# Optimization experiments

Hardware: AMD Instinct MI355X
Metric: run time of the kernel (lower is better)

The kernel has to match this reference:

```python
import math
import jax, jax.numpy as jnp
import numpy as np

B, S, D, H, F = 2, 2048, 1024, 16, 4096
HD = D // H
EPS = 1e-6
ALPHA, BETA = 0.5, 1.0  # SpectralActivation defaults


def setup_inputs() -> dict:
    key = jax.random.key(0)
    ks = jax.random.split(key, 24)
    init = lambda k, shape: (jax.random.normal(k, shape, jnp.float32) * 0.02)
    return {
        "x": jax.random.normal(ks[0], (B, S, D), jnp.float32),
        # attention params (W stored as [in, out], i.e. y = x @ W + b)
        "Wq": init(ks[1], (D, D)), "bq": jnp.zeros((D,), jnp.float32),
        "Wk": init(ks[2], (D, D)), "bk": jnp.zeros((D,), jnp.float32),
        "Wv": init(ks[3], (D, D)), "bv": jnp.zeros((D,), jnp.float32),
        "Wo": init(ks[4], (D, D)), "bo": jnp.zeros((D,), jnp.float32),
        "resonance": jnp.ones((H, 1, 1), jnp.float32),
        "phase": jnp.zeros((H, 1, 1), jnp.float32),
        # norm1
        "g1": jnp.ones((D,), jnp.float32), "b1": jnp.zeros((D,), jnp.float32),
        "s1": jnp.full((1,), 0.1, jnp.float32),
        # FFN
        "W1": init(ks[5], (D, F)), "bf1": jnp.zeros((F,), jnp.float32),
        "W2": init(ks[6], (F, D)), "bf2": jnp.zeros((D,), jnp.float32),
        # norm2
        "g2": jnp.ones((D,), jnp.float32), "b2": jnp.zeros((D,), jnp.float32),
        "s2": jnp.full((1,), 0.1, jnp.float32),
    }


def _harmonic_ln(x, gamma, beta, stab):
    mean = jnp.mean(x, axis=-1, keepdims=True)
    std = jnp.std(x, axis=-1, keepdims=True, ddof=1)  # torch std is unbiased
    std = std + stab * jnp.sin(std * math.pi)
    return gamma * ((x - mean) / (std + EPS)) + beta


def _spectral_act(x):
    c = math.sqrt(2.0 / math.pi)
    gelu_like = 0.5 * x * (1.0 + jnp.tanh(c * (x + 0.044715 * x ** 3)))
    return gelu_like + ALPHA * jnp.sin(BETA * x)


def _forward(x, Wq, bq, Wk, bk, Wv, bv, Wo, bo, resonance, phase,
             g1, b1, s1, W1, bf1, W2, bf2, g2, b2, s2):
    Bq, Sq, _ = x.shape
    q = (x @ Wq + bq).reshape(Bq, Sq, H, HD).transpose(0, 2, 1, 3)  # [B,H,S,hd]
    k = (x @ Wk + bk).reshape(Bq, Sq, H, HD).transpose(0, 2, 1, 3)
    v = (x @ Wv + bv).reshape(Bq, Sq, H, HD).transpose(0, 2, 1, 3)

    scores = jnp.einsum('bhqd,bhkd->bhqk', q, k) / math.sqrt(HD)  # [B,H,S,S]
    scores = scores + resonance[None] * jnp.sin(scores + phase[None])
    attn = jax.nn.softmax(scores, axis=-1)
    out = jnp.einsum('bhqk,bhkd->bhqd', attn, v)
    out = out.transpose(0, 2, 1, 3).reshape(Bq, Sq, D)
    attn_out = out @ Wo + bo

    x = _harmonic_ln(x + attn_out, g1, b1, s1)
    ff = _spectral_act(x @ W1 + bf1) @ W2 + bf2
    x = _harmonic_ln(x + ff, g2, b2, s2)
    return x


def reference(x, Wq, bq, Wk, bk, Wv, bv, Wo, bo, resonance, phase,
              g1, b1, s1, W1, bf1, W2, bf2, g2, b2, s2):
    return _forward(x, Wq, bq, Wk, bk, Wv, bv, Wo, bo, resonance, phase,
                    g1, b1, s1, W1, bf1, W2, bf2, g2, b2, s2)
```

## Files before the change

### kernel.cpp

```cpp
#include <hip/hip_runtime.h>
#include <cstdint>
#include <cstddef>


typedef float  f32x4  __attribute__((ext_vector_type(4)));
typedef __bf16 bf16x8 __attribute__((ext_vector_type(8)));
typedef unsigned short u16x8 __attribute__((ext_vector_type(8)));
typedef unsigned short u16x4 __attribute__((ext_vector_type(4)));
typedef unsigned int   u32x2 __attribute__((ext_vector_type(2)));
typedef unsigned int   u32x4 __attribute__((ext_vector_type(4)));

#define MFMA_BF16(a, b, c) __builtin_amdgcn_mfma_f32_16x16x32_bf16((a), (b), (c), 0, 0, 0)

static __device__ __forceinline__ unsigned short f32_to_bf16(float f) {
  return __builtin_bit_cast(unsigned short, (__bf16)f);
}
static __device__ __forceinline__ bf16x8 lds_frag(const unsigned short* base, int byte) {
  return __builtin_bit_cast(bf16x8, *(const u16x8*)((const char*)base + byte));
}
static __device__ __forceinline__ float spectral_act(float x) {
  const float c = 0.7978845608028654f;
  float g = 0.5f * x * (1.0f + tanhf(c * (x + 0.044715f * x * x * x)));
  return g + 0.5f * __sinf(x);
}
static __device__ __forceinline__ void gload_lds16(const void* g, void* lds) {
  __builtin_amdgcn_global_load_lds((const __attribute__((address_space(1))) unsigned int*)g,
                                   (__attribute__((address_space(3))) unsigned int*)lds,
                                   16, 0, 0);
}
static __device__ __forceinline__ u32x2 tr_read(unsigned addr) {
  u32x2 r;
  asm volatile("ds_read_b64_tr_b16 %0, %1" : "=v"(r) : "v"(addr));
  return r;
}

__global__ __launch_bounds__(256) void cvt_f32_bf16(const float* __restrict__ in,
                                                    unsigned short* __restrict__ out, int n) {
  int i = (blockIdx.x * 256 + threadIdx.x) * 4;
  if (i < n) {
    float4 v = *(const float4*)(in + i);
    u16x4 o;
    o[0] = f32_to_bf16(v.x); o[1] = f32_to_bf16(v.y);
    o[2] = f32_to_bf16(v.z); o[3] = f32_to_bf16(v.w);
    *(u16x4*)(out + i) = o;
  }
}

__global__ __launch_bounds__(256) void transpose_f32_bf16(const float* __restrict__ W,
                                                          unsigned short* __restrict__ Wt,
                                                          int K, int N) {
  __shared__ float tile[32][33];
  int tx = threadIdx.x & 31, ty = threadIdx.x >> 5;
  int k0 = blockIdx.y * 32, n0 = blockIdx.x * 32;
#pragma unroll
  for (int i = 0; i < 4; i++)
    tile[ty + i * 8][tx] = W[(size_t)(k0 + ty + i * 8) * N + n0 + tx];
  __syncthreads();
#pragma unroll
  for (int i = 0; i < 4; i++)
    Wt[(size_t)(n0 + ty + i * 8) * K + k0 + tx] = f32_to_bf16(tile[tx][ty + i * 8]);
}

template <int BM, int BN, int EPI>
__global__ __launch_bounds__(256) void gemm_bt(const unsigned short* __restrict__ A,
                                               const unsigned short* __restrict__ Bt,
                                               const float* __restrict__ bias,
                                               unsigned short* __restrict__ Cb,
                                               float* __restrict__ Cf,
                                               int M, int N, int K) {
  constexpr int MI = BM / 32;
  constexpr int NI = BN / 32;
  __shared__ unsigned short As[2][BM * 32];
  __shared__ unsigned short Bs[2][BN * 32];
  const int t = threadIdx.x;
  const int lane = t & 63, w = t >> 6;
  const int wr = w >> 1, wc = w & 1;
  const int g = lane >> 4, cc = lane & 15;
  const int row0 = blockIdx.y * BM, col0 = blockIdx.x * BN;

  f32x4 acc[MI][NI];
#pragma unroll
  for (int mi = 0; mi < MI; mi++)
#pragma unroll
    for (int ni = 0; ni < NI; ni++) acc[mi][ni] = (f32x4){0.f, 0.f, 0.f, 0.f};

  const int nk = K >> 5;
  const int srow = lane >> 2;
  const int schunk = (lane & 3) ^ (srow & 3);

  auto stage = [&](int buf, int kt) {
#pragma unroll
    for (int i = 0; i < BM / 64; ++i) {
      int r = i * 64 + w * 16;
      gload_lds16(A + (size_t)(row0 + r + srow) * K + (kt << 5) + schunk * 8,
                  &As[buf][r * 32]);
    }
#pragma unroll
    for (int i = 0; i < BN / 64; ++i) {
      int r = i * 64 + w * 16;
      gload_lds16(Bt + (size_t)(col0 + r + srow) * K + (kt << 5) + schunk * 8,
                  &Bs[buf][r * 32]);
    }
  };

  stage(0, 0);
  __syncthreads();
  int cur = 0;
  for (int kt = 0; kt < nk; ++kt) {
    if (kt + 1 < nk) stage(cur ^ 1, kt + 1);

    bf16x8 af[MI], bg[NI];
#pragma unroll
    for (int mi = 0; mi < MI; mi++) {
      int r = wr * (BM / 2) + mi * 16 + cc;
      af[mi] = lds_frag(&As[cur][0], r * 64 + ((g ^ (cc & 3)) << 4));
    }
#pragma unroll
    for (int ni = 0; ni < NI; ni++) {
      int r = wc * (BN / 2) + ni * 16 + cc;
      bg[ni] = lds_frag(&Bs[cur][0], r * 64 + ((g ^ (cc & 3)) << 4));
    }
#pragma unroll
    for (int mi = 0; mi < MI; mi++)
#pragma unroll
      for (int ni = 0; ni < NI; ni++)
        acc[mi][ni] = MFMA_BF16(af[mi], bg[ni], acc[mi][ni]);

    __syncthreads();
    cur ^= 1;
  }

#pragma unroll
  for (int mi = 0; mi < MI; mi++) {
#pragma unroll
    for (int ni = 0; ni < NI; ni++) {
      int col = col0 + wc * (BN / 2) + ni * 16 + cc;
      float bv = bias[col];
#pragma unroll
      for (int r4 = 0; r4 < 4; r4++) {
        int row = row0 + wr * (BM / 2) + mi * 16 + g * 4 + r4;
        float val = acc[mi][ni][r4] + bv;
        if (EPI == 2) val = spectral_act(val);
        if (EPI == 0 || EPI == 2) Cb[(size_t)row * N + col] = f32_to_bf16(val);
        else                      Cf[(size_t)row * N + col] = val;
      }
    }
  }
}

__global__ __launch_bounds__(256) void attn_fused(const unsigned short* __restrict__ Qb,
                                                  const unsigned short* __restrict__ Kb,
                                                  const unsigned short* __restrict__ Vb,
                                                  int ld,
                                                  const float* __restrict__ resonance,
                                                  const float* __restrict__ phase,
                                                  unsigned short* __restrict__ O, int ldo) {
  constexpr int S = 2048;
  __shared__ unsigned short Ks[64 * 64];
  __shared__ unsigned short Vs[4][64 * 16];
  __shared__ unsigned short Ps[4][16 * 64];

  const int t = threadIdx.x, lane = t & 63, w = t >> 6;
  const int g = lane >> 4, cc = lane & 15;
  const int bh = blockIdx.y, b = bh >> 4, h = bh & 15;
  const int q0 = blockIdx.x * 64 + w * 16;
  const float res = resonance[h], ph = phase[h];

  const unsigned short* Qh = Qb + (size_t)b * S * ld + h * 64;
  const unsigned short* Kh = Kb + (size_t)b * S * ld + h * 64;
  const unsigned short* Vh = Vb + (size_t)b * S * ld + h * 64;

  bf16x8 qa0, qa1;
  {
    const unsigned short* qp = Qh + (size_t)(q0 + cc) * ld + g * 8;
    qa0 = __builtin_bit_cast(bf16x8, *(const u16x8*)qp);
    qa1 = __builtin_bit_cast(bf16x8, *(const u16x8*)(qp + 32));
  }

  bf16x8 ones8;
#pragma unroll
  for (int j = 0; j < 8; j++) ones8[j] = (__bf16)1.0f;

  const int krow = t >> 3, kc8 = (t & 7) * 8;
  const int vkey = t & 63, vb0 = (t >> 6) * 16;
  u16x8 kr0, kr1, vr0, vr1;

  auto issue_loads = [&](int kt) {
    const unsigned short* kp = Kh + (size_t)(kt * 64) * ld;
    kr0 = *(const u16x8*)(kp + (size_t)krow * ld + kc8);
    kr1 = *(const u16x8*)(kp + (size_t)(krow + 32) * ld + kc8);
    const unsigned short* vp = Vh + (size_t)(kt * 64 + vkey) * ld + vb0;
    vr0 = *(const u16x8*)vp;
    vr1 = *(const u16x8*)(vp + 8);
  };
  auto stage_lds = [&]() {
    *(u16x8*)((char*)Ks + ((krow * 128 + kc8 * 2) ^ ((krow & 7) << 4))) = kr0;
    int row2 = krow + 32;
    *(u16x8*)((char*)Ks + ((row2 * 128 + kc8 * 2) ^ ((row2 & 7) << 4))) = kr1;
    int sw = (vkey >> 3) & 1;
    char* vb = (char*)&Vs[t >> 6][0] + vkey * 32;
    *(u16x8*)(vb + sw * 16) = vr0;
    *(u16x8*)(vb + (1 - sw) * 16) = vr1;
  };

  const unsigned vs_base = (unsigned)(uintptr_t)(void*)&Vs[0][0];
  const unsigned tr_a = vs_base + (unsigned)((8 * g + (cc >> 2)) * 32 +
                                             (((cc & 2) >> 1) ^ (g & 1)) * 16 +
                                             (cc & 1) * 8);

  f32x4 oacc[4];
#pragma unroll
  for (int i = 0; i < 4; i++) oacc[i] = (f32x4){0.f, 0.f, 0.f, 0.f};
  float Mx[4] = {-1e30f, -1e30f, -1e30f, -1e30f};
  float Lx[4] = {0.f, 0.f, 0.f, 0.f};
  char* PsW = (char*)&Ps[w][0];

  issue_loads(0);
  for (int kt = 0; kt < S / 64; ++kt) {
    stage_lds();
    __syncthreads();
    if (kt + 1 < S / 64) issue_loads(kt + 1);

    f32x4 sacc[4];
#pragma unroll
    for (int nb = 0; nb < 4; nb++) sacc[nb] = (f32x4){0.f, 0.f, 0.f, 0.f};
#pragma unroll
    for (int nb = 0; nb < 4; nb++) {
      int key = nb * 16 + cc;
      int rb = key * 128, xr = (key & 7) << 4;
      bf16x8 k0 = lds_frag(Ks, (rb + g * 16) ^ xr);
      bf16x8 k1 = lds_frag(Ks, (rb + 64 + g * 16) ^ xr);
      sacc[nb] = MFMA_BF16(qa0, k0, sacc[nb]);
      sacc[nb] = MFMA_BF16(qa1, k1, sacc[nb]);
    }

    float sm[4] = {-1e30f, -1e30f, -1e30f, -1e30f};
#pragma unroll
    for (int nb = 0; nb < 4; nb++)
#pragma unroll
      for (int r4 = 0; r4 < 4; r4++) {
        float sv = sacc[nb][r4] * 0.125f;
        sv += res * __sinf(sv + ph);
        sacc[nb][r4] = sv;
        sm[r4] = fmaxf(sm[r4], sv);
      }
#pragma unroll
    for (int d = 1; d < 16; d <<= 1)
#pragma unroll
      for (int r4 = 0; r4 < 4; r4++) sm[r4] = fmaxf(sm[r4], __shfl_xor(sm[r4], d, 16));

    float alpha[4];
#pragma unroll
    for (int r4 = 0; r4 < 4; r4++) {
      float nm = fmaxf(Mx[r4], sm[r4]);
      alpha[r4] = __expf(Mx[r4] - nm);
      Mx[r4] = nm;
    }
#pragma unroll
    for (int nb = 0; nb < 4; nb++)
#pragma unroll
      for (int r4 = 0; r4 < 4; r4++) {
        float p = __expf(sacc[nb][r4] - Mx[r4]);
        int prow = g * 4 + r4, pcol = nb * 16 + cc;
        *(unsigned short*)(PsW + ((prow * 128 + pcol * 2) ^ ((prow & 7) << 4))) =
            f32_to_bf16(p);
      }

    bf16x8 pa0, pa1;
    {
      int xr = (cc & 7) << 4;
      pa0 = lds_frag((const unsigned short*)PsW, (cc * 128 + g * 16) ^ xr);
      pa1 = lds_frag((const unsigned short*)PsW, (cc * 128 + 64 + g * 16) ^ xr);
    }
    f32x4 pacc = (f32x4){0.f, 0.f, 0.f, 0.f};
    pacc = MFMA_BF16(pa0, ones8, pacc);
    pacc = MFMA_BF16(pa1, ones8, pacc);
#pragma unroll
    for (int r4 = 0; r4 < 4; r4++) Lx[r4] = Lx[r4] * alpha[r4] + pacc[r4];
#pragma unroll
    for (int nb2 = 0; nb2 < 4; nb2++)
#pragma unroll
      for (int r4 = 0; r4 < 4; r4++) oacc[nb2][r4] *= alpha[r4];

    u32x2 trv[4][4];
#pragma unroll
    for (int b2 = 0; b2 < 4; b2++) {
      unsigned a = tr_a + b2 * 2048;
      trv[b2][0] = tr_read(a);
      trv[b2][1] = tr_read(a + 128);
      trv[b2][2] = tr_read(a + 1024);
      trv[b2][3] = tr_read(a + 1152);
    }
    asm volatile("s_waitcnt lgkmcnt(0)" ::: "memory");
    __builtin_amdgcn_sched_barrier(0);
#pragma unroll
    for (int b2 = 0; b2 < 4; b2++) {
      bf16x8 v0 = __builtin_bit_cast(bf16x8,
          (u32x4){trv[b2][0][0], trv[b2][0][1], trv[b2][1][0], trv[b2][1][1]});
      bf16x8 v1 = __builtin_bit_cast(bf16x8,
          (u32x4){trv[b2][2][0], trv[b2][2][1], trv[b2][3][0], trv[b2][3][1]});
      oacc[b2] = MFMA_BF16(pa0, v0, oacc[b2]);
      oacc[b2] = MFMA_BF16(pa1, v1, oacc[b2]);
    }
    __syncthreads();
  }

#pragma unroll
  for (int nb2 = 0; nb2 < 4; nb2++)
#pragma unroll
    for (int r4 = 0; r4 < 4; r4++) {
      float ov = oacc[nb2][r4] / Lx[r4];
      O[(size_t)(b * S + q0 + g * 4 + r4) * ldo + h * 64 + nb2 * 16 + cc] = f32_to_bf16(ov);
    }
}

__global__ __launch_bounds__(256) void resid_harmonic_ln(const float* __restrict__ xin,
                                                         const float* __restrict__ radd,
                                                         const float* __restrict__ gamma,
                                                         const float* __restrict__ beta,
                                                         const float* __restrict__ stab,
                                                         float* __restrict__ yf,
                                                         unsigned short* __restrict__ yb) {
  const int row = blockIdx.x, t = threadIdx.x;
  const float* xr = xin + (size_t)row * 1024;
  const float* rr = radd + (size_t)row * 1024;
  float v[4], s = 0.f, ss = 0.f;
#pragma unroll
  for (int j = 0; j < 4; j++) {
    int idx = t + j * 256;
    v[j] = xr[idx] + rr[idx];
    s += v[j]; ss += v[j] * v[j];
  }
#pragma unroll
  for (int d = 1; d < 64; d <<= 1) { s += __shfl_xor(s, d); ss += __shfl_xor(ss, d); }
  __shared__ float sb[8];
  int lane = t & 63, wid = t >> 6;
  if (lane == 0) { sb[wid] = s; sb[4 + wid] = ss; }
  __syncthreads();
  s = sb[0] + sb[1] + sb[2] + sb[3];
  ss = sb[4] + sb[5] + sb[6] + sb[7];
  float mean = s * (1.f / 1024.f);
  float var = fmaxf((ss - 1024.f * mean * mean) * (1.f / 1023.f), 0.f);
  float sd = sqrtf(var);
  sd += stab[0] * sinf(sd * 3.14159265358979323846f);
  float inv = 1.f / (sd + 1e-6f);
#pragma unroll
  for (int j = 0; j < 4; j++) {
    int idx = t + j * 256;
    float y = gamma[idx] * ((v[j] - mean) * inv) + beta[idx];
    yf[(size_t)row * 1024 + idx] = y;
    if (yb) yb[(size_t)row * 1024 + idx] = f32_to_bf16(y);
  }
}

extern "C" void kernel_launch(void* const* d_in, const int* in_sizes, int n_in,
                              void* d_out, int out_size, void* d_ws, size_t ws_size,
                              hipStream_t stream) {
  const float* x    = (const float*)d_in[0];
  const float* Wq   = (const float*)d_in[1];
  const float* bq   = (const float*)d_in[2];
  const float* Wk   = (const float*)d_in[3];
  const float* bk   = (const float*)d_in[4];
  const float* Wv   = (const float*)d_in[5];
  const float* bv   = (const float*)d_in[6];
  const float* Wo   = (const float*)d_in[7];
  const float* bo   = (const float*)d_in[8];
  const float* reso = (const float*)d_in[9];
  const float* phas = (const float*)d_in[10];
  const float* g1   = (const float*)d_in[11];
  const float* b1   = (const float*)d_in[12];
  const float* s1   = (const float*)d_in[13];
  const float* W1   = (const float*)d_in[14];
  const float* bf1  = (const float*)d_in[15];
  const float* W2   = (const float*)d_in[16];
  const float* bf2  = (const float*)d_in[17];
  const float* g2   = (const float*)d_in[18];
  const float* b2   = (const float*)d_in[19];
  const float* s2   = (const float*)d_in[20];

  const int BS = 4096;

  char* ws = (char*)d_ws;
  const size_t OFF_QKV  = 0;
  const size_t OFF_XB   = 25165824;
  const size_t OFF_WQKV = 33554432;
  const size_t OFF_WOT  = 39845888;
  const size_t OFF_W1T  = 41943040;
  const size_t OFF_W2T  = 50331648;
  const size_t OFF_BQKV = 58720256;
  const size_t OFF_T0   = 58736640;
  const size_t OFF_X1   = 75513856;
  const size_t OFF_X1B  = 92291072;

  unsigned short* qkv   = (unsigned short*)(ws + OFF_QKV);
  unsigned short* xb    = (unsigned short*)(ws + OFF_XB);
  unsigned short* ao    = (unsigned short*)(ws + OFF_XB);
  unsigned short* Wqkvt = (unsigned short*)(ws + OFF_WQKV);
  unsigned short* Wot   = (unsigned short*)(ws + OFF_WOT);
  unsigned short* W1t   = (unsigned short*)(ws + OFF_W1T);
  unsigned short* W2t   = (unsigned short*)(ws + OFF_W2T);
  float*          bqkv  = (float*)(ws + OFF_BQKV);
  float*          t0    = (float*)(ws + OFF_T0);
  float*          x1    = (float*)(ws + OFF_X1);
  unsigned short* x1b   = (unsigned short*)(ws + OFF_X1B);
  unsigned short* hb    = (unsigned short*)(ws + OFF_QKV);
  float*          out   = (float*)d_out;

  cvt_f32_bf16<<<4096, 256, 0, stream>>>(x, xb, BS * 1024);

  transpose_f32_bf16<<<dim3(32, 32), 256, 0, stream>>>(Wq, Wqkvt, 1024, 1024);
  transpose_f32_bf16<<<dim3(32, 32), 256, 0, stream>>>(Wk, Wqkvt + (size_t)1024 * 1024, 1024, 1024);
  transpose_f32_bf16<<<dim3(32, 32), 256, 0, stream>>>(Wv, Wqkvt + (size_t)2048 * 1024, 1024, 1024);
  transpose_f32_bf16<<<dim3(32, 32), 256, 0, stream>>>(Wo, Wot, 1024, 1024);
  transpose_f32_bf16<<<dim3(128, 32), 256, 0, stream>>>(W1, W1t, 1024, 4096);
  transpose_f32_bf16<<<dim3(32, 128), 256, 0, stream>>>(W2, W2t, 4096, 1024);

  hipMemcpyAsync((void*)bqkv,          (const void*)bq, 1024 * 4, hipMemcpyDeviceToDevice, stream);
  hipMemcpyAsync((void*)(bqkv + 1024), (const void*)bk, 1024 * 4, hipMemcpyDeviceToDevice, stream);
  hipMemcpyAsync((void*)(bqkv + 2048), (const void*)bv, 1024 * 4, hipMemcpyDeviceToDevice, stream);

  gemm_bt<128, 128, 0><<<dim3(24, 32), 256, 0, stream>>>(xb, Wqkvt, bqkv, qkv, nullptr,
                                                         4096, 3072, 1024);

  attn_fused<<<dim3(32, 32), 256, 0, stream>>>(qkv, qkv + 1024, qkv + 2048, 3072,
                                               reso, phas, ao, 1024);

  gemm_bt<128, 64, 1><<<dim3(16, 32), 256, 0, stream>>>(ao, Wot, bo, nullptr, t0,
                                                        4096, 1024, 1024);

  resid_harmonic_ln<<<4096, 256, 0, stream>>>(x, t0, g1, b1, s1, x1, x1b);

  gemm_bt<128, 128, 2><<<dim3(32, 32), 256, 0, stream>>>(x1b, W1t, bf1, hb, nullptr,
                                                         4096, 4096, 1024);

  gemm_bt<128, 64, 1><<<dim3(16, 32), 256, 0, stream>>>(hb, W2t, bf2, nullptr, t0,
                                                        4096, 1024, 4096);

  resid_harmonic_ln<<<4096, 256, 0, stream>>>(x1, t0, g2, b2, s2, out, nullptr);
}
```

Before: 488.7 us.

## Add 256x256-tile 512-thread bf16 GEMM for QKV and FFN1 projections

Introduces a new GEMM kernel with 256x256 output tiles, K-step 64, 8 waves per block, XOR-swizzled LDS layout fed by direct global-to-LDS loads, double buffering and raised wave priority around the MFMA bursts. It replaces the 128x128 kernel for the QKV projection and the FFN up-projection (with the fused spectral activation). The aim is higher arithmetic intensity per LDS byte and fewer global loads per FLOP. In exchange, the grids shrink to 192 and 256 blocks, which may leave CUs idle or give a single wave of work. The 128 KB LDS footprint also allows only one block per CU.

```diff
diff --git a/kernel.cpp b/kernel.cpp
--- a/kernel.cpp
+++ b/kernel.cpp
@@ -59,6 +59,122 @@
 #pragma unroll
   for (int i = 0; i < 4; i++)
     Wt[(size_t)(n0 + ty + i * 8) * K + k0 + tx] = f32_to_bf16(tile[tx][ty + i * 8]);
+}
+
+template <int EPI>
+__global__ __launch_bounds__(512, 2) void gemm_bt8(const unsigned short* __restrict__ Ag,
+                                                   const unsigned short* __restrict__ Bt,
+                                                   const float* __restrict__ bias,
+                                                   unsigned short* __restrict__ Cb,
+                                                   float* __restrict__ Cf,
+                                                   int M, int N, int K) {
+  __shared__ unsigned short As[2][256 * 64];
+  __shared__ unsigned short Bs[2][256 * 64];
+  const int t = threadIdx.x;
+  const int lane = t & 63, w = t >> 6;
+  const int wr = w >> 2, wc = w & 3;
+  const int g = lane >> 4, cc = lane & 15;
+  const int row0 = blockIdx.y * 256, col0 = blockIdx.x * 256;
+
+  f32x4 acc[8][4];
+#pragma unroll
+  for (int mi = 0; mi < 8; mi++)
+#pragma unroll
+    for (int ni = 0; ni < 4; ni++) acc[mi][ni] = (f32x4){0.f, 0.f, 0.f, 0.f};
+
+  const int nk = K >> 6;
+
+  const int sro = w * 8 + (lane >> 3);
+  const int sc8 = ((lane & 7) ^ ((lane >> 3) & 7)) * 8;
+
+  auto stage = [&](int buf, int kt) {
+#pragma unroll
+    for (int i = 0; i < 4; ++i) {
+      int r = i * 64 + sro;
+      gload_lds16(Ag + (size_t)(row0 + r) * K + (kt << 6) + sc8,
+                  &As[buf][(i * 64 + w * 8) * 64]);
+    }
+#pragma unroll
+    for (int i = 0; i < 4; ++i) {
+      int r = i * 64 + sro;
+      gload_lds16(Bt + (size_t)(col0 + r) * K + (kt << 6) + sc8,
+                  &Bs[buf][(i * 64 + w * 8) * 64]);
+    }
+  };
+
+  stage(0, 0);
+  if (nk > 1) {
+    stage(1, 1);
+    asm volatile("s_waitcnt vmcnt(8)" ::: "memory");
+  } else {
+    asm volatile("s_waitcnt vmcnt(0)" ::: "memory");
+  }
+  asm volatile("s_barrier" ::: "memory");
+
+  int cur = 0;
+  for (int kt = 0; kt < nk; ++kt) {
+#pragma unroll
+    for (int qm = 0; qm < 2; ++qm) {
+      bf16x8 a[2][4];
+#pragma unroll
+      for (int ks = 0; ks < 2; ++ks)
+#pragma unroll
+        for (int i = 0; i < 4; ++i) {
+          int r = wr * 128 + (qm * 4 + i) * 16 + cc;
+          a[ks][i] = lds_frag(&As[cur][0], r * 128 + (((ks * 4 + g) ^ (cc & 7)) << 4));
+        }
+#pragma unroll
+      for (int qn = 0; qn < 2; ++qn) {
+        bf16x8 bb[2][2];
+#pragma unroll
+        for (int ks = 0; ks < 2; ++ks)
+#pragma unroll
+          for (int j = 0; j < 2; ++j) {
+            int r = wc * 64 + (qn * 2 + j) * 16 + cc;
+            bb[ks][j] = lds_frag(&Bs[cur][0], r * 128 + (((ks * 4 + g) ^ (cc & 7)) << 4));
+          }
+        __builtin_amdgcn_s_setprio(1);
+#pragma unroll
+        for (int ks = 0; ks < 2; ++ks)
+#pragma unroll
+          for (int i = 0; i < 4; ++i)
+#pragma unroll
+            for (int j = 0; j < 2; ++j)
+              acc[qm * 4 + i][qn * 2 + j] =
+                  MFMA_BF16(a[ks][i], bb[ks][j], acc[qm * 4 + i][qn * 2 + j]);
+        __builtin_amdgcn_s_setprio(0);
+      }
+    }
+    if (kt == nk - 1) break;
+    asm volatile("s_waitcnt lgkmcnt(0)" ::: "memory");
+    __builtin_amdgcn_sched_barrier(0);
+    asm volatile("s_barrier" ::: "memory");
+    if (kt + 2 < nk) {
+      stage(cur, kt + 2);
+      asm volatile("s_waitcnt vmcnt(8)" ::: "memory");
+    } else {
+      asm volatile("s_waitcnt vmcnt(0)" ::: "memory");
+    }
+    asm volatile("s_barrier" ::: "memory");
+    cur ^= 1;
+  }
+
+#pragma unroll
+  for (int mi = 0; mi < 8; ++mi) {
+#pragma unroll
+    for (int ni = 0; ni < 4; ++ni) {
+      int col = col0 + wc * 64 + ni * 16 + cc;
+      float bv = bias[col];
+#pragma unroll
+      for (int r4 = 0; r4 < 4; r4++) {
+        int row = row0 + wr * 128 + mi * 16 + g * 4 + r4;
+        float val = acc[mi][ni][r4] + bv;
+        if (EPI == 2) val = spectral_act(val);
+        if (EPI == 0 || EPI == 2) Cb[(size_t)row * N + col] = f32_to_bf16(val);
+        else                      Cf[(size_t)row * N + col] = val;
+      }
+    }
+  }
 }
 
 template <int BM, int BN, int EPI>
@@ -419,8 +535,8 @@
   hipMemcpyAsync((void*)(bqkv + 1024), (const void*)bk, 1024 * 4, hipMemcpyDeviceToDevice, stream);
   hipMemcpyAsync((void*)(bqkv + 2048), (const void*)bv, 1024 * 4, hipMemcpyDeviceToDevice, stream);
 
-  gemm_bt<128, 128, 0><<<dim3(24, 32), 256, 0, stream>>>(xb, Wqkvt, bqkv, qkv, nullptr,
-                                                         4096, 3072, 1024);
+  gemm_bt8<0><<<dim3(12, 16), 512, 0, stream>>>(xb, Wqkvt, bqkv, qkv, nullptr,
+                                                4096, 3072, 1024);
 
   attn_fused<<<dim3(32, 32), 256, 0, stream>>>(qkv, qkv + 1024, qkv + 2048, 3072,
                                                reso, phas, ao, 1024);
@@ -430,8 +546,8 @@
 
   resid_harmonic_ln<<<4096, 256, 0, stream>>>(x, t0, g1, b1, s1, x1, x1b);
 
-  gemm_bt<128, 128, 2><<<dim3(32, 32), 256, 0, stream>>>(x1b, W1t, bf1, hb, nullptr,
-                                                         4096, 4096, 1024);
+  gemm_bt8<2><<<dim3(16, 16), 512, 0, stream>>>(x1b, W1t, bf1, hb, nullptr,
+                                                4096, 4096, 1024);
 
   gemm_bt<128, 64, 1><<<dim3(16, 32), 256, 0, stream>>>(hb, W2t, bf2, nullptr, t0,
                                                         4096, 1024, 4096);
```

New measurement: 505.0 us. 1.03x slower.
